# Performance work log

Hardware: AMD Instinct MI355X
Metric: run time of the kernel (lower is better)

Reference implementation:

```python
import jax, jax.numpy as jnp
import numpy as np

SCALE = np.sqrt(512.0).astype(np.float32)  # sqrt(embedding_dim)


def setup_inputs() -> dict:
    key = jax.random.key(0)
    ks = jax.random.split(key, 7)
    B, d, L = 4, 512, 4096
    num_cats, num_labels = 1168, 8929
    s = 1.0 / np.sqrt(d)
    return {
        "H": jax.random.normal(ks[0], (B, d, L), jnp.float32),
        "Wk": jax.random.normal(ks[1], (d, d), jnp.float32) * s,
        "bk": jnp.full((d,), 0.01, jnp.float32),
        "Wv": jax.random.normal(ks[2], (d, d), jnp.float32) * s,
        "bv": jnp.full((d,), 0.01, jnp.float32),
        "Q1": jax.random.normal(ks[3], (num_cats, d), jnp.float32) * s,
        "Q2": jax.random.normal(ks[4], (num_labels, d), jnp.float32) * s,
        "code2cat_map": jax.random.randint(ks[5], (num_labels,), 0, num_cats, jnp.int32),
    }


def reference(H, Wk, bk, Wv, bv, Q1, Q2, code2cat_map):
    # H: [B, d, L]; 1x1 Conv1d == per-position linear, then ELU, then permute -> [B, L, d]
    K = jax.nn.elu(jnp.einsum('bfl,df->bld', H, Wk) + bk)  # [B, L, d]
    V = jax.nn.elu(jnp.einsum('bfl,df->bld', H, Wv) + bv)  # [B, L, d]
    # Stage 1: category-level attention
    E1 = jnp.einsum('cd,bld->bcl', Q1, K) / SCALE           # [B, C1, L]
    A1 = jax.nn.softmax(E1, axis=-1)
    C1 = jnp.einsum('bcl,bld->bcd', A1, V)                  # [B, C1, d]
    # Per-code gather-add context injection (replaces the Python loop)
    Q2b = Q2[None, :, :] + C1[:, code2cat_map, :]           # [B, Lbl, d]
    # Stage 2: label-level attention
    E2 = jnp.einsum('bnd,bld->bnl', Q2b, K) / SCALE          # [B, Lbl, L]
    A2 = jax.nn.softmax(E2, axis=-1)
    C2 = jnp.einsum('bnl,bld->bnd', A2, V)                   # [B, Lbl, d]
    return (C2, A2)
```

## Files before the change

### kernel.cpp

```cpp
#include <hip/hip_runtime.h>


#define RSCALE 0.04419417382415922f

typedef __attribute__((ext_vector_type(8))) short bf16x8;
typedef __attribute__((ext_vector_type(4))) float f32x4;

__device__ __forceinline__ ushort f2bf(float x) {
  union { float f; unsigned u; } c; c.f = x;
  unsigned u = c.u;
  return (ushort)((u + 0x7fffu + ((u >> 16) & 1u)) >> 16);
}

__device__ __forceinline__ void gl_lds16(const ushort* g, ushort* l) {
  __builtin_amdgcn_global_load_lds(
      (const __attribute__((address_space(1))) unsigned*)g,
      (__attribute__((address_space(3))) unsigned*)l, 16, 0, 0);
}

template <int EPI>
__global__ __launch_bounds__(256) void gemm_bt(
    const ushort* __restrict__ A, const ushort* __restrict__ B,
    void* __restrict__ Cv, const float* __restrict__ bias,
    int M, int N, int K, long long sA, long long sB, long long sC) {
  __shared__ ushort ldsA[128 * 32];
  __shared__ ushort ldsB[128 * 32];
  const int tid = threadIdx.x;
  const int wave = tid >> 6, lane = tid & 63;
  const int m0 = blockIdx.y * 128, n0 = blockIdx.x * 128;
  const int z = blockIdx.z;
  A += (size_t)z * sA;
  B += (size_t)z * sB;

  const int lr = lane >> 2;
  const int lcol = (lane & 3) * 8;
  int rA0 = m0 + wave * 16 + lr;      if (rA0 > M - 1) rA0 = M - 1;
  int rA1 = m0 + 64 + wave * 16 + lr; if (rA1 > M - 1) rA1 = M - 1;
  const int rB0 = n0 + wave * 16 + lr;
  const int rB1 = n0 + 64 + wave * 16 + lr;
  const ushort* pA0 = A + (size_t)rA0 * K + lcol;
  const ushort* pA1 = A + (size_t)rA1 * K + lcol;
  const ushort* pB0 = B + (size_t)rB0 * K + lcol;
  const ushort* pB1 = B + (size_t)rB1 * K + lcol;
  ushort* dA0 = ldsA + wave * 512;
  ushort* dA1 = ldsA + 2048 + wave * 512;
  ushort* dB0 = ldsB + wave * 512;
  ushort* dB1 = ldsB + 2048 + wave * 512;

  const int wm = (wave >> 1) * 64, wn = (wave & 1) * 64;
  const ushort* aBase = ldsA + (wm + (lane & 15)) * 32 + (lane >> 4) * 8;
  const ushort* bBase = ldsB + (wn + (lane & 15)) * 32 + (lane >> 4) * 8;

  f32x4 acc[4][4];
  f32x4 z4 = {0.f, 0.f, 0.f, 0.f};
#pragma unroll
  for (int i = 0; i < 4; i++)
#pragma unroll
    for (int j = 0; j < 4; j++) acc[i][j] = z4;

  for (int k0 = 0; k0 < K; k0 += 32) {
    __syncthreads();
    gl_lds16(pA0 + k0, dA0);
    gl_lds16(pA1 + k0, dA1);
    gl_lds16(pB0 + k0, dB0);
    gl_lds16(pB1 + k0, dB1);
    __syncthreads();
    bf16x8 af[4], bv[4];
#pragma unroll
    for (int i = 0; i < 4; i++) af[i] = *(const bf16x8*)(aBase + i * 512);
#pragma unroll
    for (int i = 0; i < 4; i++) bv[i] = *(const bf16x8*)(bBase + i * 512);
#pragma unroll
    for (int mi = 0; mi < 4; mi++)
#pragma unroll
      for (int ni = 0; ni < 4; ni++)
        acc[mi][ni] = __builtin_amdgcn_mfma_f32_16x16x32_bf16(
            af[mi], bv[ni], acc[mi][ni], 0, 0, 0);
  }

  const int cc = lane & 15;
  const int cr = (lane >> 4) * 4;
  float* Cf = (float*)Cv + (size_t)z * sC;
  ushort* Cb = (ushort*)Cv + (size_t)z * sC;
#pragma unroll
  for (int mi = 0; mi < 4; mi++) {
#pragma unroll
    for (int ni = 0; ni < 4; ni++) {
      const int col = n0 + wn + ni * 16 + cc;
#pragma unroll
      for (int r = 0; r < 4; r++) {
        const int row = m0 + wm + mi * 16 + cr + r;
        if (row < M) {
          float x = acc[mi][ni][r];
          if (EPI == 0) {
            Cf[(size_t)row * N + col] = x;
          } else if (EPI == 1) {
            Cf[(size_t)row * N + col] = x * RSCALE;
          } else {
            x += bias[col];
            x = x > 0.f ? x : (__expf(x) - 1.f);
            Cb[(size_t)row * N + col] = f2bf(x);
          }
        }
      }
    }
  }
}

__global__ __launch_bounds__(256) void softmax_rows(const float* X, float* Yf,
                                                    ushort* __restrict__ Ybf) {
  const size_t row = blockIdx.x;
  const int tid = threadIdx.x;
  const float4* xr = (const float4*)(X + row * 4096);
  float4 v[4];
  float m = -3.4e38f;
#pragma unroll
  for (int i = 0; i < 4; i++) {
    v[i] = xr[tid + 256 * i];
    m = fmaxf(m, fmaxf(fmaxf(v[i].x, v[i].y), fmaxf(v[i].z, v[i].w)));
  }
#pragma unroll
  for (int o = 32; o >= 1; o >>= 1) m = fmaxf(m, __shfl_xor(m, o));
  __shared__ float sred[4];
  __shared__ float sred2[4];
  const int wave = tid >> 6, lane = tid & 63;
  if (lane == 0) sred[wave] = m;
  __syncthreads();
  m = fmaxf(fmaxf(sred[0], sred[1]), fmaxf(sred[2], sred[3]));
  float4 e[4];
  float s = 0.f;
#pragma unroll
  for (int i = 0; i < 4; i++) {
    e[i].x = __expf(v[i].x - m);
    e[i].y = __expf(v[i].y - m);
    e[i].z = __expf(v[i].z - m);
    e[i].w = __expf(v[i].w - m);
    s += e[i].x + e[i].y + e[i].z + e[i].w;
  }
#pragma unroll
  for (int o = 32; o >= 1; o >>= 1) s += __shfl_xor(s, o);
  if (lane == 0) sred2[wave] = s;
  __syncthreads();
  s = sred2[0] + sred2[1] + sred2[2] + sred2[3];
  const float inv = 1.f / s;
  float4* yf = Yf ? (float4*)(Yf + row * 4096) : nullptr;
  ushort4* yb = (ushort4*)(Ybf + row * 4096);
#pragma unroll
  for (int i = 0; i < 4; i++) {
    float4 w;
    w.x = e[i].x * inv; w.y = e[i].y * inv;
    w.z = e[i].z * inv; w.w = e[i].w * inv;
    if (yf) yf[tid + 256 * i] = w;
    ushort4 u;
    u.x = f2bf(w.x); u.y = f2bf(w.y); u.z = f2bf(w.z); u.w = f2bf(w.w);
    yb[tid + 256 * i] = u;
  }
}

__global__ __launch_bounds__(256) void transpose_f32_bf16(
    const float* __restrict__ src, ushort* __restrict__ dst, int R, int C) {
  __shared__ float t[32][33];
  const size_t boff = (size_t)blockIdx.z * R * C;
  const int r0 = blockIdx.y * 32, c0 = blockIdx.x * 32;
  const int tx = threadIdx.x & 31, ty = threadIdx.x >> 5;
#pragma unroll
  for (int j = ty; j < 32; j += 8)
    t[j][tx] = src[boff + (size_t)(r0 + j) * C + c0 + tx];
  __syncthreads();
#pragma unroll
  for (int j = ty; j < 32; j += 8)
    dst[boff + (size_t)(c0 + j) * R + r0 + tx] = f2bf(t[tx][j]);
}

__global__ __launch_bounds__(256) void transpose_u16(
    const ushort* __restrict__ src, ushort* __restrict__ dst, int R, int C) {
  __shared__ ushort t[32][33];
  const size_t boff = (size_t)blockIdx.z * R * C;
  const int r0 = blockIdx.y * 32, c0 = blockIdx.x * 32;
  const int tx = threadIdx.x & 31, ty = threadIdx.x >> 5;
#pragma unroll
  for (int j = ty; j < 32; j += 8)
    t[j][tx] = src[boff + (size_t)(r0 + j) * C + c0 + tx];
  __syncthreads();
#pragma unroll
  for (int j = ty; j < 32; j += 8)
    dst[boff + (size_t)(c0 + j) * R + r0 + tx] = t[tx][j];
}

__global__ __launch_bounds__(256) void cvt_f32_bf16_k(
    const float* __restrict__ s, ushort* __restrict__ dst, int n4) {
  const int t = blockIdx.x * 256 + threadIdx.x;
  if (t >= n4) return;
  const float4 v = ((const float4*)s)[t];
  ushort4 o;
  o.x = f2bf(v.x); o.y = f2bf(v.y); o.z = f2bf(v.z); o.w = f2bf(v.w);
  ((ushort4*)dst)[t] = o;
}

__global__ __launch_bounds__(256) void build_q2b(
    const float* __restrict__ Q2, const float* __restrict__ C1,
    const int* __restrict__ cmap, ushort* __restrict__ out) {
  const long long t = (long long)blockIdx.x * 256 + threadIdx.x;
  if (t >= 4LL * 8929 * 128) return;
  const int c4 = (int)(t & 127);
  const long long rowid = t >> 7;
  const int n = (int)(rowid % 8929);
  const int b = (int)(rowid / 8929);
  const float4 q = ((const float4*)(Q2 + (size_t)n * 512))[c4];
  const int cat = cmap[n];
  const float4 c = ((const float4*)(C1 + ((size_t)b * 1168 + cat) * 512))[c4];
  ushort4 o;
  o.x = f2bf(q.x + c.x); o.y = f2bf(q.y + c.y);
  o.z = f2bf(q.z + c.z); o.w = f2bf(q.w + c.w);
  ((ushort4*)(out + ((size_t)b * 8929 + n) * 512))[c4] = o;
}

extern "C" void kernel_launch(void* const* d_in, const int* in_sizes, int n_in,
                              void* d_out, int out_size, void* d_ws,
                              size_t ws_size, hipStream_t stream) {
  const float* H = (const float*)d_in[0];
  const float* Wk = (const float*)d_in[1];
  const float* bk = (const float*)d_in[2];
  const float* Wv = (const float*)d_in[3];
  const float* bv = (const float*)d_in[4];
  const float* Q1 = (const float*)d_in[5];
  const float* Q2 = (const float*)d_in[6];
  const int* cmap = (const int*)d_in[7];

  const int Bn = 4, d = 512, L = 4096, C1n = 1168, NL = 8929;

  char* w = (char*)d_ws;
  size_t off = 0;
  auto alloc = [&](size_t bytes) { void* p = w + off; off += bytes; return p; };
  ushort* Hb  = (ushort*)alloc((size_t)Bn * L * d * 2);
  ushort* Kb  = (ushort*)alloc((size_t)Bn * L * d * 2);
  ushort* Vb  = (ushort*)alloc((size_t)Bn * L * d * 2);
  ushort* Vt  = (ushort*)alloc((size_t)Bn * d * L * 2);
  ushort* Wkb = (ushort*)alloc((size_t)d * d * 2);
  ushort* Wvb = (ushort*)alloc((size_t)d * d * 2);
  ushort* Q1b = (ushort*)alloc((size_t)C1n * d * 2);
  ushort* A1b = (ushort*)alloc((size_t)Bn * C1n * L * 2);
  float*  C1  = (float*)alloc((size_t)Bn * C1n * d * 4);
  ushort* Q2b = (ushort*)alloc((size_t)Bn * NL * d * 2);
  float*  E1  = (float*)(w + off);
  ushort* A2b = (ushort*)(w + off);
  const size_t e1B = (size_t)Bn * C1n * L * 4;
  const size_t a2bPer = (size_t)NL * L * 2;
  int nb = 1;
  if (ws_size >= off + (a2bPer * 4 > e1B ? a2bPer * 4 : e1B)) nb = 4;
  else if (ws_size >= off + (a2bPer * 2 > e1B ? a2bPer * 2 : e1B)) nb = 2;

  float* C2out = (float*)d_out;
  float* A2out = (float*)d_out + (size_t)Bn * NL * d;

  cvt_f32_bf16_k<<<dim3((d * d / 4 + 255) / 256), 256, 0, stream>>>(Wk, Wkb, d * d / 4);
  cvt_f32_bf16_k<<<dim3((d * d / 4 + 255) / 256), 256, 0, stream>>>(Wv, Wvb, d * d / 4);
  cvt_f32_bf16_k<<<dim3((C1n * d / 4 + 255) / 256), 256, 0, stream>>>(Q1, Q1b, C1n * d / 4);
  transpose_f32_bf16<<<dim3(L / 32, d / 32, Bn), 256, 0, stream>>>(H, Hb, d, L);
  gemm_bt<2><<<dim3(d / 128, (Bn * L) / 128, 1), 256, 0, stream>>>(
      Hb, Wkb, Kb, bk, Bn * L, d, d, 0, 0, 0);
  gemm_bt<2><<<dim3(d / 128, (Bn * L) / 128, 1), 256, 0, stream>>>(
      Hb, Wvb, Vb, bv, Bn * L, d, d, 0, 0, 0);
  transpose_u16<<<dim3(d / 32, L / 32, Bn), 256, 0, stream>>>(Vb, Vt, L, d);
  gemm_bt<1><<<dim3(L / 128, (C1n + 127) / 128, Bn), 256, 0, stream>>>(
      Q1b, Kb, E1, nullptr, C1n, L, d, 0, (long long)L * d, (long long)C1n * L);
  softmax_rows<<<dim3(Bn * C1n), 256, 0, stream>>>(E1, nullptr, A1b);
  gemm_bt<0><<<dim3(d / 128, (C1n + 127) / 128, Bn), 256, 0, stream>>>(
      A1b, Vt, C1, nullptr, C1n, d, L, (long long)C1n * L, (long long)d * L,
      (long long)C1n * d);
  build_q2b<<<dim3(17858), 256, 0, stream>>>(Q2, C1, cmap, Q2b);

  for (int g = 0; g < Bn / nb; ++g) {
    const ushort* Qg = Q2b + (size_t)g * nb * NL * d;
    const ushort* Kg = Kb + (size_t)g * nb * L * d;
    const ushort* Vtg = Vt + (size_t)g * nb * d * L;
    float* Eg = A2out + (size_t)g * nb * NL * L;
    float* Cg = C2out + (size_t)g * nb * NL * d;
    gemm_bt<1><<<dim3(L / 128, (NL + 127) / 128, nb), 256, 0, stream>>>(
        Qg, Kg, Eg, nullptr, NL, L, d, (long long)NL * d, (long long)L * d,
        (long long)NL * L);
    softmax_rows<<<dim3(nb * NL), 256, 0, stream>>>(Eg, Eg, A2b);
    gemm_bt<0><<<dim3(d / 128, (NL + 127) / 128, nb), 256, 0, stream>>>(
        A2b, Vtg, Cg, nullptr, NL, d, L, (long long)NL * L, (long long)d * L,
        (long long)NL * d);
  }
}
```

Baseline: 1.698 ms.

## Add 256x256-tile 8-wave GEMM with triple-buffered LDS for label scores

Adds a new GEMM kernel with 512 threads that computes a 256x256 output tile per block. It uses a three-stage LDS ring fed by direct global-to-LDS loads, with prefetch two k-steps ahead, and raises wave priority around the MFMA bursts. It replaces the 128x128 kernel only for the stage-2 score GEMM (Q2b x K^T), to increase operand reuse per byte loaded and to hide load latency. The cost is higher register pressure from 32 accumulators per wave plus 96KB of LDS per block, and more padded rows in the last tile along the label dimension.

```diff
diff --git a/kernel.cpp b/kernel.cpp
--- a/kernel.cpp
+++ b/kernel.cpp
@@ -90,6 +90,144 @@
 #pragma unroll
       for (int r = 0; r < 4; r++) {
         const int row = m0 + wm + mi * 16 + cr + r;
+        if (row < M) {
+          float x = acc[mi][ni][r];
+          if (EPI == 0) {
+            Cf[(size_t)row * N + col] = x;
+          } else if (EPI == 1) {
+            Cf[(size_t)row * N + col] = x * RSCALE;
+          } else {
+            x += bias[col];
+            x = x > 0.f ? x : (__expf(x) - 1.f);
+            Cb[(size_t)row * N + col] = f2bf(x);
+          }
+        }
+      }
+    }
+  }
+}
+
+template <int EPI>
+__global__ __launch_bounds__(512, 2) void gemm8_bt(
+    const ushort* __restrict__ A, const ushort* __restrict__ B,
+    void* __restrict__ Cv, const float* __restrict__ bias,
+    int M, int N, int K, long long sA, long long sB, long long sC) {
+  __shared__ ushort lds[3 * 16384];
+  const int tid = threadIdx.x;
+  const int wave = tid >> 6, lane = tid & 63;
+  const int m0 = blockIdx.y * 256, n0 = blockIdx.x * 256;
+  const int z = blockIdx.z;
+  A += (size_t)z * sA;
+  B += (size_t)z * sB;
+
+  const int srow = wave * 16 + (lane >> 2);
+  const int scol = ((lane & 3) ^ ((lane >> 3) & 3)) * 8;
+  int rA0 = m0 + srow;        if (rA0 > M - 1) rA0 = M - 1;
+  int rA1 = m0 + 128 + srow;  if (rA1 > M - 1) rA1 = M - 1;
+  int rB0 = n0 + srow;        if (rB0 > N - 1) rB0 = N - 1;
+  int rB1 = n0 + 128 + srow;  if (rB1 > N - 1) rB1 = N - 1;
+  const ushort* pA0 = A + (size_t)rA0 * K + scol;
+  const ushort* pA1 = A + (size_t)rA1 * K + scol;
+  const ushort* pB0 = B + (size_t)rB0 * K + scol;
+  const ushort* pB1 = B + (size_t)rB1 * K + scol;
+  const int wbase = wave * 512;
+
+  const int wmi = wave >> 2;
+  const int wni = wave & 3;
+  const int li = lane & 15;
+  const int slotx = (((lane >> 4) ^ ((li >> 1) & 3)) * 8);
+  const int aOff = (wmi * 128 + li) * 32 + slotx;
+  const int bOff = 8192 + (wni * 64 + li) * 32 + slotx;
+
+  f32x4 acc[8][4];
+  f32x4 z4 = {0.f, 0.f, 0.f, 0.f};
+#pragma unroll
+  for (int i = 0; i < 8; i++)
+#pragma unroll
+    for (int j = 0; j < 4; j++) acc[i][j] = z4;
+
+  {
+    ushort* b0 = lds;
+    gl_lds16(pA0, b0 + wbase);
+    gl_lds16(pA1, b0 + 4096 + wbase);
+    gl_lds16(pB0, b0 + 8192 + wbase);
+    gl_lds16(pB1, b0 + 12288 + wbase);
+    ushort* b1 = lds + 16384;
+    gl_lds16(pA0 + 32, b1 + wbase);
+    gl_lds16(pA1 + 32, b1 + 4096 + wbase);
+    gl_lds16(pB0 + 32, b1 + 8192 + wbase);
+    gl_lds16(pB1 + 32, b1 + 12288 + wbase);
+  }
+  asm volatile("s_waitcnt vmcnt(4)" ::: "memory");
+  __builtin_amdgcn_s_barrier();
+  __builtin_amdgcn_sched_barrier(0);
+
+  const int NT = K >> 5;
+  int bsel = 0, nsel = 2;
+  for (int t = 0; t < NT; ++t) {
+    const ushort* cur = lds + bsel * 16384;
+    ushort* nxt = lds + nsel * 16384;
+    const bool pf = (t + 2) < NT;
+    const int kpf = (t + 2) << 5;
+    if (pf) {
+      gl_lds16(pA0 + kpf, nxt + wbase);
+      gl_lds16(pA1 + kpf, nxt + 4096 + wbase);
+    }
+    bf16x8 af[4], bfr[4];
+#pragma unroll
+    for (int mi = 0; mi < 4; mi++)
+      af[mi] = *(const bf16x8*)(cur + aOff + mi * 512);
+#pragma unroll
+    for (int ni = 0; ni < 4; ni++)
+      bfr[ni] = *(const bf16x8*)(cur + bOff + ni * 512);
+    __builtin_amdgcn_s_setprio(1);
+#pragma unroll
+    for (int mi = 0; mi < 4; mi++)
+#pragma unroll
+      for (int ni = 0; ni < 4; ni++)
+        acc[mi][ni] = __builtin_amdgcn_mfma_f32_16x16x32_bf16(
+            af[mi], bfr[ni], acc[mi][ni], 0, 0, 0);
+    __builtin_amdgcn_s_setprio(0);
+    if (pf) {
+      gl_lds16(pB0 + kpf, nxt + 8192 + wbase);
+      gl_lds16(pB1 + kpf, nxt + 12288 + wbase);
+    }
+    bf16x8 af2[4];
+#pragma unroll
+    for (int mi = 0; mi < 4; mi++)
+      af2[mi] = *(const bf16x8*)(cur + aOff + 2048 + mi * 512);
+    __builtin_amdgcn_s_setprio(1);
+#pragma unroll
+    for (int mi = 0; mi < 4; mi++)
+#pragma unroll
+      for (int ni = 0; ni < 4; ni++)
+        acc[mi + 4][ni] = __builtin_amdgcn_mfma_f32_16x16x32_bf16(
+            af2[mi], bfr[ni], acc[mi + 4][ni], 0, 0, 0);
+    __builtin_amdgcn_s_setprio(0);
+    asm volatile("s_waitcnt lgkmcnt(0)" ::: "memory");
+    if (pf) {
+      asm volatile("s_waitcnt vmcnt(4)" ::: "memory");
+    } else {
+      asm volatile("s_waitcnt vmcnt(0)" ::: "memory");
+    }
+    __builtin_amdgcn_s_barrier();
+    __builtin_amdgcn_sched_barrier(0);
+    bsel = (bsel == 2) ? 0 : bsel + 1;
+    nsel = (nsel == 2) ? 0 : nsel + 1;
+  }
+
+  const int cc = lane & 15;
+  const int cr = (lane >> 4) * 4;
+  float* Cf = (float*)Cv + (size_t)z * sC;
+  ushort* Cb = (ushort*)Cv + (size_t)z * sC;
+#pragma unroll
+  for (int mi = 0; mi < 8; mi++) {
+#pragma unroll
+    for (int ni = 0; ni < 4; ni++) {
+      const int col = n0 + wni * 64 + ni * 16 + cc;
+#pragma unroll
+      for (int r = 0; r < 4; r++) {
+        const int row = m0 + wmi * 128 + mi * 16 + cr + r;
         if (row < M) {
           float x = acc[mi][ni][r];
           if (EPI == 0) {
@@ -276,7 +414,7 @@
     const ushort* Vtg = Vt + (size_t)g * nb * d * L;
     float* Eg = A2out + (size_t)g * nb * NL * L;
     float* Cg = C2out + (size_t)g * nb * NL * d;
-    gemm_bt<1><<<dim3(L / 128, (NL + 127) / 128, nb), 256, 0, stream>>>(
+    gemm8_bt<1><<<dim3(L / 256, (NL + 255) / 256, nb), 512, 0, stream>>>(
         Qg, Kg, Eg, nullptr, NL, L, d, (long long)NL * d, (long long)L * d,
         (long long)NL * L);
     softmax_rows<<<dim3(nb * NL), 256, 0, stream>>>(Eg, Eg, A2b);
```

Result: faster. 1.663 ms (-2.0%).
